# Performance work log

Hardware: AMD Instinct MI355X
Metric: run time of the kernel (lower is better)

## Reference

```python
import jax, jax.numpy as jnp
import numpy as np

HEADS = 8
DIM = 32  # dim_heads


def setup_inputs() -> dict:
    key = jax.random.key(0)
    k1, k2, k3, k4 = jax.random.split(key, 4)
    b, c, h, w = 8, 256, 128, 128
    hidden = HEADS * DIM  # 256
    x = jax.random.normal(k1, (b, c, h, w), dtype=jnp.float32)
    w_qkv = jax.random.normal(k2, (3 * hidden, c), dtype=jnp.float32) * 0.05
    w_out = jax.random.normal(k3, (c, hidden), dtype=jnp.float32) * 0.05
    b_out = jax.random.normal(k4, (c,), dtype=jnp.float32) * 0.05
    return {"x": x, "w_qkv": w_qkv, "w_out": w_out, "b_out": b_out}


def reference(x, w_qkv, w_out, b_out):
    b, c, h, w = x.shape
    n = h * w
    # 1x1 conv == channel matmul: [b, 3*heads*dim, h, w]
    qkv = jnp.einsum('bchw,oc->bohw', x, w_qkv)
    # rearrange 'b (qkv heads c) h w -> qkv b heads c (h w)'
    qkv = qkv.reshape(b, 3, HEADS, DIM, n)
    q, k, v = qkv[:, 0], qkv[:, 1], qkv[:, 2]  # each [b, heads, dim, n]
    k = jax.nn.softmax(k, axis=-1)
    # context: [b, heads, dim, dim]
    context = jnp.einsum('bhdn,bhen->bhde', k, v)
    o = jnp.einsum('bhde,bhdn->bhen', context, q)  # [b, heads, dim, n]
    o = o.reshape(b, HEADS * DIM, h, w)
    # out 1x1 conv with bias
    o = jnp.einsum('bchw,oc->bohw', o, w_out) + b_out[None, :, None, None]
    return o
```

## Files before the change

kernel.cpp:

```cpp
#include <hip/hip_runtime.h>
#include <hip/hip_bf16.h>
#include <cstdint>

#define NPIX 16384
#define BATCH 8
#define CDIM 256
#define MQKV 768

typedef __bf16 bh8 __attribute__((ext_vector_type(8)));
typedef __bf16 bh4 __attribute__((ext_vector_type(4)));
typedef float  fx4 __attribute__((ext_vector_type(4)));

__device__ __forceinline__ void gload16(const void* g, void* l) {
  __builtin_amdgcn_global_load_lds(
      (const __attribute__((address_space(1))) uint32_t*)g,
      (__attribute__((address_space(3))) uint32_t*)l, 16, 0, 0);
}

__device__ __forceinline__ fx4 mfma16(bh8 a, bh8 b, fx4 c) {
  return __builtin_amdgcn_mfma_f32_16x16x32_bf16(a, b, c, 0, 0, 0);
}

__device__ __forceinline__ void pbar() {
  asm volatile("" ::: "memory");
  __builtin_amdgcn_s_barrier();
  asm volatile("" ::: "memory");
}
#define VMWI(n) asm volatile("s_waitcnt vmcnt(" #n ")" ::: "memory")

__global__ void conv_w(const float* __restrict__ w, __bf16* __restrict__ wb, int n) {
  int i = blockIdx.x * 256 + threadIdx.x;
  if (i < n) wb[i] = (__bf16)w[i];
}

__global__ __launch_bounds__(256) void transpose_wq(const float* __restrict__ w_qkv,
                                                    __bf16* __restrict__ wqT) {
  __shared__ float tile[32][33];
  const int t0 = blockIdx.x * 32, o0 = blockIdx.y * 32;
  const int tx = threadIdx.x & 31, ty = threadIdx.x >> 5;
#pragma unroll
  for (int j = 0; j < 4; ++j) {
    int r = ty * 4 + j;
    tile[r][tx] = w_qkv[(size_t)(o0 + r) * 256 + t0 + tx];
  }
  __syncthreads();
#pragma unroll
  for (int j = 0; j < 4; ++j) {
    int tl = ty * 4 + j;
    wqT[(size_t)(t0 + tl) * 256 + o0 + tx] = (__bf16)tile[tx][tl];
  }
}

__global__ __launch_bounds__(256) void transpose_x(const float* __restrict__ x,
                                                   __bf16* __restrict__ xT) {
  __shared__ float tf[64][33];
  const int n0 = blockIdx.x * 32, c0 = blockIdx.y * 64, b = blockIdx.z;
  const int u = threadIdx.x;
  const int tx = u & 31, tg = u >> 5;
#pragma unroll
  for (int j = 0; j < 8; ++j) {
    int r = tg * 8 + j;
    tf[r][tx] = x[((size_t)b * CDIM + c0 + r) * NPIX + n0 + tx];
  }
  __syncthreads();
  const int nl = u >> 3, cl = (u & 7) * 8;
  bh8 v;
#pragma unroll
  for (int j = 0; j < 8; ++j) v[j] = (__bf16)tf[cl + j][nl];
  *(bh8*)&xT[((size_t)b * NPIX + n0 + nl) * CDIM + c0 + cl] = v;
}


#define BSP(pb) ((__bf16*)(smem + 32768 + (pb)*16384))

#define STA(kt)                                                                \
  do {                                                                         \
    _Pragma("unroll") for (int i_ = 0; i_ < 4; ++i_) {                         \
      int j_ = i_ * 512 + tid;                                                 \
      int row_ = j_ >> 3, c_ = j_ & 7;                                         \
      int sc_ = c_ ^ (row_ & 7);                                               \
      gload16(Ab + (size_t)row_ * 256 + (kt)*64 + sc_ * 8, As + j_ * 8);       \
    }                                                                          \
  } while (0)

#define STB(kt, pb)                                                            \
  do {                                                                         \
    _Pragma("unroll") for (int i_ = 0; i_ < 2; ++i_) {                         \
      int j_ = i_ * 512 + tid;                                                 \
      int row_ = j_ >> 3, c_ = j_ & 7;                                         \
      int sc_ = c_ ^ (row_ & 7);                                               \
      gload16(Bb + (size_t)row_ * 256 + (kt)*64 + sc_ * 8, BSP(pb) + j_ * 8);  \
    }                                                                          \
  } while (0)

#define COMP(pb)                                                               \
  do {                                                                         \
    _Pragma("unroll") for (int ks_ = 0; ks_ < 2; ++ks_) {                      \
      bh8 a_[4], b_[4];                                                        \
      const int swk_ = (ks_ * 4 + fq) ^ (fr & 7);                              \
      _Pragma("unroll") for (int m_ = 0; m_ < 4; ++m_)                         \
        a_[m_] = *(const bh8*)&As[(wm * 64 + m_ * 16 + fr) * 64 + swk_ * 8];   \
      _Pragma("unroll") for (int n_ = 0; n_ < 4; ++n_)                         \
        b_[n_] = *(const bh8*)&BSP(pb)[(wn * 64 + n_ * 16 + fr) * 64 + swk_ * 8];\
      _Pragma("unroll") for (int m_ = 0; m_ < 4; ++m_)                         \
      _Pragma("unroll") for (int n_ = 0; n_ < 4; ++n_)                         \
        acc[m_][n_] = mfma16(a_[m_], b_[n_], acc[m_][n_]);                     \
    }                                                                          \
  } while (0)

template <int EPI>
__global__ __launch_bounds__(512, 4) void gemm256(
    const __bf16* __restrict__ A, const __bf16* __restrict__ Bx,
    __bf16* __restrict__ ekmat, __bf16* __restrict__ vmat,
    const float* __restrict__ bias, float* __restrict__ fout) {
  __shared__ __align__(16) char smem[65536];
  __bf16* As = (__bf16*)smem;
  const int tid = threadIdx.x;
  const int bx = blockIdx.x, by = blockIdx.y, b = blockIdx.z;
  const int lane = tid & 63, wid = tid >> 6;
  const int wm = wid >> 1, wn = wid & 1;
  const int fr = lane & 15, fq = lane >> 4;
  const __bf16* Ab = A + (size_t)((EPI == 0) ? (1 + by) : b) * 65536;
  const __bf16* Bb = Bx + ((size_t)b * NPIX + (size_t)bx * 128) * 256;

  fx4 acc[4][4] = {};

  STB(0, 0); STA(0);
  STB(1, 1); VMWI(2); pbar(); COMP(0); pbar(); STA(1);
  STB(2, 0); VMWI(2); pbar(); COMP(1); pbar(); STA(2);
  STB(3, 1); VMWI(2); pbar(); COMP(0); pbar(); STA(3);
             VMWI(0); pbar(); COMP(1); pbar();

  if (EPI == 0) {
    __bf16* dst = (by == 0) ? ekmat : vmat;
    const size_t dbase = (size_t)b * CDIM * NPIX + (size_t)bx * 128;
    __bf16* Lh = (__bf16*)smem;
#pragma unroll
    for (int m = 0; m < 4; ++m) {
      __syncthreads();
#pragma unroll
      for (int n = 0; n < 4; ++n)
#pragma unroll
        for (int j = 0; j < 4; ++j) {
          float v = acc[m][n][j];
          if (by == 0) v = __expf(v);
          Lh[(wm * 16 + fq * 4 + j) * 136 + wn * 64 + n * 16 + fr] = (__bf16)v;
        }
      __syncthreads();
#pragma unroll
      for (int it = 0; it < 2; ++it) {
        int u = it * 512 + tid;
        int rr = u >> 4, cc = u & 15;
        int gch = (rr >> 4) * 64 + m * 16 + (rr & 15);
        bh8 val = *(const bh8*)&Lh[rr * 136 + cc * 8];
        *(bh8*)&dst[dbase + (size_t)gch * NPIX + cc * 8] = val;
      }
    }
  } else {
    const size_t obase = (size_t)b * CDIM * NPIX + (size_t)bx * 128;
    float* Ls = (float*)smem;
#pragma unroll
    for (int m = 0; m < 4; ++m) {
      __syncthreads();
#pragma unroll
      for (int n = 0; n < 4; ++n)
#pragma unroll
        for (int j = 0; j < 4; ++j)
          Ls[(wm * 16 + fq * 4 + j) * 132 + wn * 64 + n * 16 + fr] =
              acc[m][n][j] + bias[wm * 64 + m * 16 + fq * 4 + j];
      __syncthreads();
#pragma unroll
      for (int it = 0; it < 4; ++it) {
        int u = it * 512 + tid;
        int rr = u >> 5, cc = u & 31;
        int gch = (rr >> 4) * 64 + m * 16 + (rr & 15);
        fx4 val = *(const fx4*)&Ls[rr * 132 + cc * 4];
        *(fx4*)&fout[obase + (size_t)gch * NPIX + cc * 4] = val;
      }
    }
  }
}

__global__ __launch_bounds__(256) void ctx_kernel(const __bf16* __restrict__ ekmat,
                                                  const __bf16* __restrict__ vmat,
                                                  float* __restrict__ S_part,
                                                  float* __restrict__ Zpart) {
  const int chunk = blockIdx.x, h = blockIdx.y, b = blockIdx.z;
  const int t = threadIdx.x;
  const int n0 = chunk * 256;
  __shared__ __bf16 EK[32 * 256];
  __shared__ __bf16 VS[32 * 256];
  __shared__ float zrow[32];

  if (t < 32) zrow[t] = 0.f;
#pragma unroll
  for (int i = 0; i < 4; ++i) {
    int e0 = i * 2048 + t * 8;
    int row = e0 >> 8, col = e0 & 255;
    gload16(ekmat + ((size_t)b * CDIM + h * 32 + row) * NPIX + n0 + col, (void*)(EK + e0));
    gload16(vmat  + ((size_t)b * CDIM + h * 32 + row) * NPIX + n0 + col, (void*)(VS + e0));
  }
  __syncthreads();

  {
    const int row = t >> 3, c0 = (t & 7) * 32;
    float zacc = 0.f;
#pragma unroll
    for (int i = 0; i < 4; ++i) {
      bh8 ev = *(const bh8*)&EK[row * 256 + c0 + i * 8];
#pragma unroll
      for (int j = 0; j < 8; ++j) zacc += (float)ev[j];
    }
    atomicAdd(&zrow[row], zacc);
  }

  const int wid = t >> 6, lane = t & 63, fr = lane & 15, fq = lane >> 4;
  fx4 acc[2][2] = {};
  const int kbase = wid * 64;
#pragma unroll
  for (int kk = 0; kk < 2; ++kk) {
    bh8 a[2], bb[2];
#pragma unroll
    for (int m = 0; m < 2; ++m)
      a[m] = *(const bh8*)&EK[(m * 16 + fr) * 256 + kbase + kk * 32 + fq * 8];
#pragma unroll
    for (int n = 0; n < 2; ++n)
      bb[n] = *(const bh8*)&VS[(n * 16 + fr) * 256 + kbase + kk * 32 + fq * 8];
#pragma unroll
    for (int m = 0; m < 2; ++m)
#pragma unroll
      for (int n = 0; n < 2; ++n) acc[m][n] = mfma16(a[m], bb[n], acc[m][n]);
  }
  __syncthreads();
  float* red = (float*)EK;
#pragma unroll
  for (int m = 0; m < 2; ++m)
#pragma unroll
    for (int n = 0; n < 2; ++n)
#pragma unroll
      for (int j = 0; j < 4; ++j)
        red[wid * 1024 + (m * 16 + fq * 4 + j) * 32 + (n * 16 + fr)] = acc[m][n][j];
  __syncthreads();
  const size_t bh = (size_t)b * 8 + h;
  for (int i = t; i < 1024; i += 256) {
    float s = red[i] + red[1024 + i] + red[2048 + i] + red[3072 + i];
    S_part[(bh * 64 + chunk) * 1024 + i] = s;
  }
  if (t < 32) Zpart[(bh * 64 + chunk) * 32 + t] = zrow[t];
}

__global__ __launch_bounds__(256) void reduce_ctx(const float* __restrict__ S_part,
                                                  const float* __restrict__ Zpart,
                                                  float* __restrict__ ctx) {
  const int bh = blockIdx.x;
  const int t = threadIdx.x;
  __shared__ float zs[32];
  if (t < 32) {
    float z = 0.f;
    for (int ch = 0; ch < 64; ++ch) z += Zpart[((size_t)bh * 64 + ch) * 32 + t];
    zs[t] = z;
  }
  __syncthreads();
  for (int i = t; i < 1024; i += 256) {
    float s = 0.f;
    for (int ch = 0; ch < 64; ++ch) s += S_part[((size_t)bh * 64 + ch) * 1024 + i];
    ctx[(size_t)bh * 1024 + i] = s / zs[i >> 5];
  }
}

__global__ __launch_bounds__(256) void make_w2(const float* __restrict__ ctx,
                                               const float* __restrict__ w_out,
                                               __bf16* __restrict__ W2b) {
  const int oc = blockIdx.x, b = blockIdx.y, t = threadIdx.x;
  const int h = t >> 5, d = t & 31;
  const float* wrow = w_out + oc * 256 + h * 32;
  const float* crow = ctx + (((size_t)b * 8 + h) * 32 + d) * 32;
  float s = 0.f;
#pragma unroll
  for (int e = 0; e < 32; ++e) s += wrow[e] * crow[e];
  W2b[((size_t)b * 256 + oc) * 256 + t] = (__bf16)s;
}

__global__ __launch_bounds__(256) void make_w3(const __bf16* __restrict__ W2b,
                                               const __bf16* __restrict__ wqT,
                                               __bf16* __restrict__ W3) {
  const int bx = blockIdx.x, by = blockIdx.y, b = blockIdx.z;
  const int lane = threadIdx.x & 63, wid = threadIdx.x >> 6;
  const int wm = wid >> 1, wn = wid & 1;
  const int fr = lane & 15, fq = lane >> 4;
  const __bf16* Ab = W2b + (size_t)b * 65536 + (size_t)(by * 128 + wm * 64) * 256;
  const __bf16* Bb = wqT + (size_t)(bx * 128 + wn * 64) * 256;
  fx4 acc[4][4] = {};
#pragma unroll
  for (int h = 0; h < 8; ++h) {
    bh8 a_[4], b_[4];
#pragma unroll
    for (int m = 0; m < 4; ++m)
      a_[m] = *(const bh8*)(Ab + (size_t)(m * 16 + fr) * 256 + h * 32 + fq * 8);
#pragma unroll
    for (int n = 0; n < 4; ++n)
      b_[n] = *(const bh8*)(Bb + (size_t)(n * 16 + fr) * 256 + h * 32 + fq * 8);
#pragma unroll
    for (int m = 0; m < 4; ++m)
#pragma unroll
      for (int n = 0; n < 4; ++n) acc[m][n] = mfma16(a_[m], b_[n], acc[m][n]);
  }
#pragma unroll
  for (int m = 0; m < 4; ++m)
#pragma unroll
    for (int n = 0; n < 4; ++n) {
      int r0 = by * 128 + wm * 64 + m * 16 + fq * 4;
      int t0 = bx * 128 + wn * 64 + n * 16 + fr;
#pragma unroll
      for (int j = 0; j < 4; ++j)
        W3[(size_t)b * 65536 + (size_t)(r0 + j) * 256 + t0] = (__bf16)acc[m][n][j];
    }
}

extern "C" void kernel_launch(void* const* d_in, const int* in_sizes, int n_in,
                              void* d_out, int out_size, void* d_ws, size_t ws_size,
                              hipStream_t stream) {
  const float* x     = (const float*)d_in[0];
  const float* w_qkv = (const float*)d_in[1];
  const float* w_out = (const float*)d_in[2];
  const float* b_out = (const float*)d_in[3];
  float* out = (float*)d_out;

  char* ws = (char*)d_ws;
  __bf16* xT    = (__bf16*)(ws);
  __bf16* wqb   = (__bf16*)(ws + 67108864ull);
  __bf16* wqT   = (__bf16*)(ws + 67502080ull);
  __bf16* W2b   = (__bf16*)(ws + 67633152ull);
  __bf16* W3    = (__bf16*)(ws + 68681728ull);
  float*  S_part= (float*) (ws + 69730304ull);
  float*  Zpart = (float*) (ws + 86507520ull);
  float*  ctx   = (float*) (ws + 87031808ull);

  __bf16* ekmat = (__bf16*)d_out;
  __bf16* vmat  = ekmat + (size_t)BATCH * CDIM * NPIX;

  conv_w<<<768, 256, 0, stream>>>(w_qkv, wqb, MQKV * CDIM);
  transpose_wq<<<dim3(8, 8), 256, 0, stream>>>(w_qkv, wqT);
  transpose_x<<<dim3(NPIX / 32, CDIM / 64, BATCH), 256, 0, stream>>>(x, xT);
  gemm256<0><<<dim3(NPIX / 128, 2, BATCH), 512, 0, stream>>>(
      wqb, xT, ekmat, vmat, nullptr, nullptr);
  ctx_kernel<<<dim3(64, 8, BATCH), 256, 0, stream>>>(ekmat, vmat, S_part, Zpart);
  reduce_ctx<<<64, 256, 0, stream>>>(S_part, Zpart, ctx);
  make_w2<<<dim3(256, BATCH), 256, 0, stream>>>(ctx, w_out, W2b);
  make_w3<<<dim3(2, 2, BATCH), 256, 0, stream>>>(W2b, wqT, W3);
  gemm256<1><<<dim3(NPIX / 128, 1, BATCH), 512, 0, stream>>>(
      W3, xT, nullptr, nullptr, b_out, out);
}
```

Measured before the change: 199.5 us.

## Fuse context computation into QKV GEMM epilogue, dropping exp(K)/V materialization

The QKV projection GEMM now computes K and V rows for the same four heads in one tile. Its epilogue applies exp to K, stages both in swizzled LDS, and computes per-tile partial K·V^T and row sums with MFMA. These are written straight to S_part and Zpart, which removes the separate ctx_kernel and the round trip of the large bf16 K/V intermediates through global memory. In exchange, the number of partial chunks doubles to 128, so reduce_ctx reads twice as much partial data. The GEMM epilogue also gets longer and uses slightly more LDS, which may lower occupancy.

```diff
diff --git a/kernel.cpp b/kernel.cpp
--- a/kernel.cpp
+++ b/kernel.cpp
@@ -5,7 +5,6 @@
 #define NPIX 16384
 #define BATCH 8
 #define CDIM 256
-#define MQKV 768
 
 typedef __bf16 bh8 __attribute__((ext_vector_type(8)));
 typedef __bf16 bh4 __attribute__((ext_vector_type(4)));
@@ -79,7 +78,11 @@
       int j_ = i_ * 512 + tid;                                                 \
       int row_ = j_ >> 3, c_ = j_ & 7;                                         \
       int sc_ = c_ ^ (row_ & 7);                                               \
-      gload16(Ab + (size_t)row_ * 256 + (kt)*64 + sc_ * 8, As + j_ * 8);       \
+      const __bf16* sb_;                                                       \
+      if (EPI == 0) sb_ = (i_ < 2) ? Abk + (size_t)row_ * 256                  \
+                                   : Abv + (size_t)(row_ - 128) * 256;         \
+      else          sb_ = Ab + (size_t)row_ * 256;                             \
+      gload16(sb_ + (kt)*64 + sc_ * 8, As + j_ * 8);                           \
     }                                                                          \
   } while (0)
 
@@ -111,16 +114,19 @@
 template <int EPI>
 __global__ __launch_bounds__(512, 4) void gemm256(
     const __bf16* __restrict__ A, const __bf16* __restrict__ Bx,
-    __bf16* __restrict__ ekmat, __bf16* __restrict__ vmat,
+    float* __restrict__ S_part, float* __restrict__ Zpart,
     const float* __restrict__ bias, float* __restrict__ fout) {
-  __shared__ __align__(16) char smem[65536];
+  __shared__ __align__(16) char smem[66560];
   __bf16* As = (__bf16*)smem;
   const int tid = threadIdx.x;
   const int bx = blockIdx.x, by = blockIdx.y, b = blockIdx.z;
   const int lane = tid & 63, wid = tid >> 6;
   const int wm = wid >> 1, wn = wid & 1;
   const int fr = lane & 15, fq = lane >> 4;
-  const __bf16* Ab = A + (size_t)((EPI == 0) ? (1 + by) : b) * 65536;
+  const int hg = by * 4;
+  const __bf16* Abk = A + (size_t)(hg * 32) * 256;
+  const __bf16* Abv = A + (size_t)(256 + hg * 32) * 256;
+  const __bf16* Ab  = A + (size_t)b * 65536;
   const __bf16* Bb = Bx + ((size_t)b * NPIX + (size_t)bx * 128) * 256;
 
   fx4 acc[4][4] = {};
@@ -132,29 +138,73 @@
              VMWI(0); pbar(); COMP(1); pbar();
 
   if (EPI == 0) {
-    __bf16* dst = (by == 0) ? ekmat : vmat;
-    const size_t dbase = (size_t)b * CDIM * NPIX + (size_t)bx * 128;
-    __bf16* Lh = (__bf16*)smem;
-#pragma unroll
-    for (int m = 0; m < 4; ++m) {
-      __syncthreads();
+    float* zrow = (float*)(smem + 65536);
+    if (tid < 128) zrow[tid] = 0.f;
+#pragma unroll
+    for (int m = 0; m < 4; ++m)
 #pragma unroll
       for (int n = 0; n < 4; ++n)
 #pragma unroll
         for (int j = 0; j < 4; ++j) {
-          float v = acc[m][n][j];
-          if (by == 0) v = __expf(v);
-          Lh[(wm * 16 + fq * 4 + j) * 136 + wn * 64 + n * 16 + fr] = (__bf16)v;
+          int r = wm * 64 + m * 16 + fq * 4 + j;
+          int px = wn * 64 + n * 16 + fr;
+          int pc = px >> 3;
+          if (wm < 2) {
+            int byo = r * 256 + ((pc ^ (r & 7)) << 4) + (px & 7) * 2;
+            *(__bf16*)(smem + byo) = (__bf16)__expf(acc[m][n][j]);
+          } else {
+            int r2 = r - 128;
+            int byo = r2 * 256 + ((pc ^ (r2 & 7)) << 4) + (px & 7) * 2;
+            *(__bf16*)(smem + 32768 + byo) = (__bf16)acc[m][n][j];
+          }
         }
-      __syncthreads();
-#pragma unroll
-      for (int it = 0; it < 2; ++it) {
-        int u = it * 512 + tid;
-        int rr = u >> 4, cc = u & 15;
-        int gch = (rr >> 4) * 64 + m * 16 + (rr & 15);
-        bh8 val = *(const bh8*)&Lh[rr * 136 + cc * 8];
-        *(bh8*)&dst[dbase + (size_t)gch * NPIX + cc * 8] = val;
+    __syncthreads();
+    {
+      int r = tid >> 2, c0 = (tid & 3) * 32;
+      float za = 0.f;
+#pragma unroll
+      for (int i2 = 0; i2 < 4; ++i2) {
+        int px0 = c0 + i2 * 8;
+        int pc = px0 >> 3;
+        bh8 ev = *(const bh8*)(smem + r * 256 + ((pc ^ (r & 7)) << 4));
+#pragma unroll
+        for (int jj = 0; jj < 8; ++jj) za += (float)ev[jj];
       }
+      atomicAdd(&zrow[r], za);
+    }
+    fx4 sac0 = {}, sac1 = {};
+#pragma unroll
+    for (int t2 = 0; t2 < 2; ++t2) {
+      int tk = wid * 2 + t2;
+      int hl = tk >> 2, quad = tk & 3;
+      int drow = (quad >> 1) * 16, erow = (quad & 1) * 16;
+      fx4 sac = {};
+#pragma unroll
+      for (int kt2 = 0; kt2 < 4; ++kt2) {
+        int ra = hl * 32 + drow + fr;
+        int rb = hl * 32 + erow + fr;
+        int pc = kt2 * 4 + fq;
+        bh8 af = *(const bh8*)(smem + ra * 256 + ((pc ^ (ra & 7)) << 4));
+        bh8 bf = *(const bh8*)(smem + 32768 + rb * 256 + ((pc ^ (rb & 7)) << 4));
+        sac = mfma16(af, bf, sac);
+      }
+      if (t2 == 0) sac0 = sac; else sac1 = sac;
+    }
+    __syncthreads();
+#pragma unroll
+    for (int t2 = 0; t2 < 2; ++t2) {
+      int tk = wid * 2 + t2;
+      int hl = tk >> 2, quad = tk & 3;
+      int drow = (quad >> 1) * 16, erow = (quad & 1) * 16;
+      float* sp = S_part + ((size_t)((b * 8 + hg + hl) * 128 + bx)) * 1024;
+      fx4 sv = (t2 == 0) ? sac0 : sac1;
+#pragma unroll
+      for (int j = 0; j < 4; ++j)
+        sp[(drow + fq * 4 + j) * 32 + erow + fr] = sv[j];
+    }
+    if (tid < 128) {
+      int head = hg + (tid >> 5);
+      Zpart[((size_t)(b * 8 + head) * 128 + bx) * 32 + (tid & 31)] = zrow[tid];
     }
   } else {
     const size_t obase = (size_t)b * CDIM * NPIX + (size_t)bx * 128;
@@ -179,74 +229,6 @@
       }
     }
   }
-}
-
-__global__ __launch_bounds__(256) void ctx_kernel(const __bf16* __restrict__ ekmat,
-                                                  const __bf16* __restrict__ vmat,
-                                                  float* __restrict__ S_part,
-                                                  float* __restrict__ Zpart) {
-  const int chunk = blockIdx.x, h = blockIdx.y, b = blockIdx.z;
-  const int t = threadIdx.x;
-  const int n0 = chunk * 256;
-  __shared__ __bf16 EK[32 * 256];
-  __shared__ __bf16 VS[32 * 256];
-  __shared__ float zrow[32];
-
-  if (t < 32) zrow[t] = 0.f;
-#pragma unroll
-  for (int i = 0; i < 4; ++i) {
-    int e0 = i * 2048 + t * 8;
-    int row = e0 >> 8, col = e0 & 255;
-    gload16(ekmat + ((size_t)b * CDIM + h * 32 + row) * NPIX + n0 + col, (void*)(EK + e0));
-    gload16(vmat  + ((size_t)b * CDIM + h * 32 + row) * NPIX + n0 + col, (void*)(VS + e0));
-  }
-  __syncthreads();
-
-  {
-    const int row = t >> 3, c0 = (t & 7) * 32;
-    float zacc = 0.f;
-#pragma unroll
-    for (int i = 0; i < 4; ++i) {
-      bh8 ev = *(const bh8*)&EK[row * 256 + c0 + i * 8];
-#pragma unroll
-      for (int j = 0; j < 8; ++j) zacc += (float)ev[j];
-    }
-    atomicAdd(&zrow[row], zacc);
-  }
-
-  const int wid = t >> 6, lane = t & 63, fr = lane & 15, fq = lane >> 4;
-  fx4 acc[2][2] = {};
-  const int kbase = wid * 64;
-#pragma unroll
-  for (int kk = 0; kk < 2; ++kk) {
-    bh8 a[2], bb[2];
-#pragma unroll
-    for (int m = 0; m < 2; ++m)
-      a[m] = *(const bh8*)&EK[(m * 16 + fr) * 256 + kbase + kk * 32 + fq * 8];
-#pragma unroll
-    for (int n = 0; n < 2; ++n)
-      bb[n] = *(const bh8*)&VS[(n * 16 + fr) * 256 + kbase + kk * 32 + fq * 8];
-#pragma unroll
-    for (int m = 0; m < 2; ++m)
-#pragma unroll
-      for (int n = 0; n < 2; ++n) acc[m][n] = mfma16(a[m], bb[n], acc[m][n]);
-  }
-  __syncthreads();
-  float* red = (float*)EK;
-#pragma unroll
-  for (int m = 0; m < 2; ++m)
-#pragma unroll
-    for (int n = 0; n < 2; ++n)
-#pragma unroll
-      for (int j = 0; j < 4; ++j)
-        red[wid * 1024 + (m * 16 + fq * 4 + j) * 32 + (n * 16 + fr)] = acc[m][n][j];
-  __syncthreads();
-  const size_t bh = (size_t)b * 8 + h;
-  for (int i = t; i < 1024; i += 256) {
-    float s = red[i] + red[1024 + i] + red[2048 + i] + red[3072 + i];
-    S_part[(bh * 64 + chunk) * 1024 + i] = s;
-  }
-  if (t < 32) Zpart[(bh * 64 + chunk) * 32 + t] = zrow[t];
 }
 
 __global__ __launch_bounds__(256) void reduce_ctx(const float* __restrict__ S_part,
@@ -257,13 +239,13 @@
   __shared__ float zs[32];
   if (t < 32) {
     float z = 0.f;
-    for (int ch = 0; ch < 64; ++ch) z += Zpart[((size_t)bh * 64 + ch) * 32 + t];
+    for (int ch = 0; ch < 128; ++ch) z += Zpart[((size_t)bh * 128 + ch) * 32 + t];
     zs[t] = z;
   }
   __syncthreads();
   for (int i = t; i < 1024; i += 256) {
     float s = 0.f;
-    for (int ch = 0; ch < 64; ++ch) s += S_part[((size_t)bh * 64 + ch) * 1024 + i];
+    for (int ch = 0; ch < 128; ++ch) s += S_part[((size_t)bh * 128 + ch) * 1024 + i];
     ctx[(size_t)bh * 1024 + i] = s / zs[i >> 5];
   }
 }
@@ -329,22 +311,18 @@
   char* ws = (char*)d_ws;
   __bf16* xT    = (__bf16*)(ws);
   __bf16* wqb   = (__bf16*)(ws + 67108864ull);
-  __bf16* wqT   = (__bf16*)(ws + 67502080ull);
-  __bf16* W2b   = (__bf16*)(ws + 67633152ull);
-  __bf16* W3    = (__bf16*)(ws + 68681728ull);
-  float*  S_part= (float*) (ws + 69730304ull);
-  float*  Zpart = (float*) (ws + 86507520ull);
-  float*  ctx   = (float*) (ws + 87031808ull);
-
-  __bf16* ekmat = (__bf16*)d_out;
-  __bf16* vmat  = ekmat + (size_t)BATCH * CDIM * NPIX;
-
-  conv_w<<<768, 256, 0, stream>>>(w_qkv, wqb, MQKV * CDIM);
+  __bf16* wqT   = (__bf16*)(ws + 67371008ull);
+  __bf16* W2b   = (__bf16*)(ws + 67502080ull);
+  __bf16* W3    = (__bf16*)(ws + 68550656ull);
+  float*  S_part= (float*) (ws + 69599232ull);
+  float*  Zpart = (float*) (ws + 103153664ull);
+  float*  ctx   = (float*) (ws + 104202240ull);
+
+  conv_w<<<512, 256, 0, stream>>>(w_qkv + 256 * 256, wqb, 512 * 256);
   transpose_wq<<<dim3(8, 8), 256, 0, stream>>>(w_qkv, wqT);
   transpose_x<<<dim3(NPIX / 32, CDIM / 64, BATCH), 256, 0, stream>>>(x, xT);
   gemm256<0><<<dim3(NPIX / 128, 2, BATCH), 512, 0, stream>>>(
-      wqb, xT, ekmat, vmat, nullptr, nullptr);
-  ctx_kernel<<<dim3(64, 8, BATCH), 256, 0, stream>>>(ekmat, vmat, S_part, Zpart);
+      wqb, xT, S_part, Zpart, nullptr, nullptr);
   reduce_ctx<<<64, 256, 0, stream>>>(S_part, Zpart, ctx);
   make_w2<<<dim3(256, BATCH), 256, 0, stream>>>(ctx, w_out, W2b);
   make_w3<<<dim3(2, 2, BATCH), 256, 0, stream>>>(W2b, wqT, W3);
```

New measurement: 192.9 us. 3.3% less time.
